# Performance work log

Hardware: AMD Instinct MI355X
Metric: run time of the kernel (lower is better)

Reference implementation:

```python
import jax, jax.numpy as jnp
import numpy as np

# WGS84 constants
_A = 6378137.0
_E2 = 6.69437999014e-3  # first eccentricity squared

ALPHA = 1.0
GAMMA = 2.0
DYNAMIC_GAMMA = True
SCALE_FACTOR = 1.0


def _geodetic_to_ecef(lat_rad, lon_rad, h):
    sl, cl = jnp.sin(lat_rad), jnp.cos(lat_rad)
    so, co = jnp.sin(lon_rad), jnp.cos(lon_rad)
    N = _A / jnp.sqrt(1.0 - _E2 * sl * sl)
    x = (N + h) * cl * co
    y = (N + h) * cl * so
    z = (N * (1.0 - _E2) + h) * sl
    return jnp.stack([x, y, z], axis=-1)


def setup_inputs() -> dict:
    key = jax.random.key(0)
    k1, k2, k3, k4 = jax.random.split(key, 4)
    B = 4_000_000
    lat = jax.random.uniform(k1, (B,), jnp.float32, -80.0, 80.0)    # degrees
    lon = jax.random.uniform(k2, (B,), jnp.float32, -180.0, 180.0)  # degrees
    h = jax.random.uniform(k3, (B,), jnp.float32, 0.0, 1000.0)      # meters
    targets = jnp.stack([lat, lon, h], axis=1)
    ref_ecef = _geodetic_to_ecef(jnp.deg2rad(lat), jnp.deg2rad(lon), h)
    # predicted ECEF = true ECEF + ~meters of noise -> realistic GNSS error
    inputs = ref_ecef + 2.0 * jax.random.normal(k4, (B, 3), jnp.float32)
    return {"inputs": inputs, "targets": targets}


def _ecef_to_enu(pred_ecef, gt_geodetic):
    # Batched version of the per-sample ecef_to_enu_torch loop.
    lat = jnp.deg2rad(gt_geodetic[:, 0])
    lon = jnp.deg2rad(gt_geodetic[:, 1])
    h = gt_geodetic[:, 2]
    ref = _geodetic_to_ecef(lat, lon, h)
    d = pred_ecef - ref  # [B,3]
    sl, cl = jnp.sin(lat), jnp.cos(lat)
    so, co = jnp.sin(lon), jnp.cos(lon)
    dx, dy, dz = d[:, 0], d[:, 1], d[:, 2]
    e = -so * dx + co * dy
    n = -sl * co * dx - sl * so * dy + cl * dz
    u = cl * co * dx + cl * so * dy + sl * dz
    return jnp.stack([e, n, u], axis=1)  # [B,3]


def reference(inputs, targets):
    enu_errors = _ecef_to_enu(inputs, targets)                 # [B,3]
    squared_dist = jnp.sqrt(jnp.sum(enu_errors * enu_errors, axis=1))  # L2 norm [B]
    base_loss = squared_dist
    if DYNAMIC_GAMMA:
        dyn_gamma = GAMMA * jnp.exp(-SCALE_FACTOR * base_loss)
    else:
        dyn_gamma = GAMMA
    focal_weight = jnp.power(1.0 - jnp.sqrt(squared_dist / (jnp.max(squared_dist) + 1e-8)), dyn_gamma)
    focal_loss = ALPHA * focal_weight * base_loss
    return jnp.sqrt(jnp.mean(focal_loss * focal_loss))
```

## Files before the change

kernel.cpp:

```cpp
#include <hip/hip_runtime.h>
#include <hip/hip_fp16.h>
#include <math.h>


#define THREADS 256
#define PART_CAP 8192
#define NB2_CAP 2048
#define BMAX_OFF 64
#define PART_OFF (64 + PART_CAP * 4)
#define DIST_OFF (1 << 20)

__device__ __forceinline__ void sincos8(const double* __restrict__ x,
                                        double* __restrict__ s,
                                        double* __restrict__ c) {
    const double TWO_OVER_PI = 0.636619772367581343076;
    const double PIO2_HI = 1.57079632679489655800e+00;
    const double PIO2_LO = 6.12323399573676603587e-17;

    double kd[8], r[8], r2[8];
    int q[8];
#pragma unroll
    for (int j = 0; j < 8; ++j) {
        kd[j] = rint(x[j] * TWO_OVER_PI);
        q[j] = ((int)kd[j]) & 3;
    }
#pragma unroll
    for (int j = 0; j < 8; ++j) {
        double rr = fma(-kd[j], PIO2_HI, x[j]);
        r[j] = fma(-kd[j], PIO2_LO, rr);
        r2[j] = r[j] * r[j];
    }
    float rf[8], psf[8], pcf[8];
#pragma unroll
    for (int j = 0; j < 8; ++j) rf[j] = (float)r2[j];
#pragma unroll
    for (int j = 0; j < 8; ++j) { psf[j] = -2.50507602534068634195e-08f;
                                  pcf[j] =  2.08757232129817482790e-09f; }
#pragma unroll
    for (int j = 0; j < 8; ++j) { psf[j] = fmaf(psf[j], rf[j],  2.75573137070700676789e-06f);
                                  pcf[j] = fmaf(pcf[j], rf[j], -2.75573143513906633035e-07f); }
#pragma unroll
    for (int j = 0; j < 8; ++j) { psf[j] = fmaf(psf[j], rf[j], -1.98412698298579493134e-04f);
                                  pcf[j] = fmaf(pcf[j], rf[j],  2.48015872894767294178e-05f); }
#pragma unroll
    for (int j = 0; j < 8; ++j) { psf[j] = fmaf(psf[j], rf[j],  8.33333333332248946124e-03f);
                                  pcf[j] = fmaf(pcf[j], rf[j], -1.38888888888741095749e-03f); }
#pragma unroll
    for (int j = 0; j < 8; ++j) {
        double ps = fma((double)psf[j], r2[j], -1.66666666666666324348e-01);
        double pc = fma((double)pcf[j], r2[j],  4.16666666666666019037e-02);
        double sv = fma(r2[j] * r[j], ps, r[j]);
        double cv = fma(r2[j] * r2[j], pc, fma(-0.5, r2[j], 1.0));
        double sr = (q[j] & 1) ? cv : sv;
        double cr = (q[j] & 1) ? sv : cv;
        s[j] = (q[j] & 2) ? -sr : sr;
        c[j] = ((q[j] + 1) & 2) ? -cr : cr;
    }
}

__device__ __forceinline__ void dist_group4(const float* __restrict__ lat,
                                            const float* __restrict__ lon,
                                            const float* __restrict__ hh,
                                            const float* __restrict__ px,
                                            const float* __restrict__ py,
                                            const float* __restrict__ pz,
                                            float* __restrict__ dout) {
    const float D2R = (float)0.017453292519943295;
    double x[8], s8[8], c8[8];
#pragma unroll
    for (int j = 0; j < 4; ++j) x[j] = (double)(lat[j] * D2R);
#pragma unroll
    for (int j = 0; j < 4; ++j) x[4 + j] = (double)(lon[j] * D2R);
    sincos8(x, s8, c8);

    const double A = 6378137.0, E2 = 0.00669437999014;
#pragma unroll
    for (int j = 0; j < 4; ++j) {
        double sl = s8[j], cl = c8[j], so = s8[4 + j], co = c8[4 + j];
        double h = (double)hh[j];
        double w = fma(-E2 * sl, sl, 1.0);
        double y0 = (double)__frsqrt_rn((float)w);
        double y = y0 * fma(-0.5 * w, y0 * y0, 1.5);
        double N = A * y, Nh = N + h;
        double X = Nh * cl * co;
        double Y = Nh * cl * so;
        double Z = fma(N, -E2, N + h) * sl;
        double dx = (double)px[j] - X;
        double dy = (double)py[j] - Y;
        double dz = (double)pz[j] - Z;
        dout[j] = sqrtf((float)(dx * dx + dy * dy + dz * dz));
    }
}

__device__ __forceinline__ float dist_one(float latd, float lond, float hf,
                                          float pxx, float pyy, float pzz) {
    float lat[4] = {latd, latd, latd, latd}, lon[4] = {lond, lond, lond, lond};
    float hh[4] = {hf, hf, hf, hf};
    float px[4] = {pxx, pxx, pxx, pxx}, py[4] = {pyy, pyy, pyy, pyy}, pz[4] = {pzz, pzz, pzz, pzz};
    float d[4];
    dist_group4(lat, lon, hh, px, py, pz, d);
    return d[0];
}

#define UNPACK4(ta, tb, tc, lat, lon, hh)                         \
    float lat[4] = {ta.x, ta.w, tb.z, tc.y};                      \
    float lon[4] = {ta.y, tb.x, tb.w, tc.z};                      \
    float hh[4]  = {ta.z, tb.y, tc.x, tc.w};

__device__ __forceinline__ void store_half4(__half* p, float d0, float d1, float d2, float d3) {
    union { __half2 h2[2]; uint2 u; } pk;
    pk.h2[0] = __floats2half2_rn(d0, d1);
    pk.h2[1] = __floats2half2_rn(d2, d3);
    *(uint2*)p = pk.u;
}

__global__ __launch_bounds__(THREADS, 3)
void k_pass1(const float* __restrict__ inp, const float* __restrict__ tgt,
             __half* __restrict__ dist_arr, float* __restrict__ blockmax, long B) {
    long ngroups = (B + 3) >> 2;
    long nthreads = (long)gridDim.x * blockDim.x;
    long gstride = 2 * nthreads;
    float lmax = 0.0f;
    for (long g = (long)blockIdx.x * blockDim.x + threadIdx.x; g < ngroups; g += gstride) {
        long gA = g;
        long gB = g + nthreads;
        long baseA = gA << 2;
        long baseB = gB << 2;
        bool fastA = (baseA + 3 < B);
        bool fastB = (gB < ngroups) && (baseB + 3 < B);

        if (fastA && fastB) {
            const float4* tA = (const float4*)(tgt + 3 * baseA);
            const float4* pA = (const float4*)(inp + 3 * baseA);
            const float4* tB = (const float4*)(tgt + 3 * baseB);
            const float4* pB = (const float4*)(inp + 3 * baseB);
            float4 ta0 = tA[0], ta1 = tA[1], ta2 = tA[2];
            float4 pa0 = pA[0], pa1 = pA[1], pa2 = pA[2];
            float4 tb0 = tB[0], tb1 = tB[1], tb2 = tB[2];
            float4 pb0 = pB[0], pb1 = pB[1], pb2 = pB[2];

            UNPACK4(ta0, ta1, ta2, latA, lonA, hhA);
            UNPACK4(pa0, pa1, pa2, pxA, pyA, pzA);
            float dA[4];
            dist_group4(latA, lonA, hhA, pxA, pyA, pzA, dA);

            UNPACK4(tb0, tb1, tb2, latB, lonB, hhB);
            UNPACK4(pb0, pb1, pb2, pxB, pyB, pzB);
            float dB[4];
            dist_group4(latB, lonB, hhB, pxB, pyB, pzB, dB);

            if (dist_arr) {
                store_half4(dist_arr + baseA, dA[0], dA[1], dA[2], dA[3]);
                store_half4(dist_arr + baseB, dB[0], dB[1], dB[2], dB[3]);
            }
            lmax = fmaxf(lmax, fmaxf(fmaxf(dA[0], dA[1]), fmaxf(dA[2], dA[3])));
            lmax = fmaxf(lmax, fmaxf(fmaxf(dB[0], dB[1]), fmaxf(dB[2], dB[3])));
        } else {
            for (int pass = 0; pass < 2; ++pass) {
                long gg = pass ? gB : gA;
                if (gg >= ngroups) continue;
                long base = gg << 2;
                long end = base + 4 < B ? base + 4 : B;
                for (long i = base; i < end; ++i) {
                    float d = dist_one(tgt[3*i], tgt[3*i+1], tgt[3*i+2],
                                       inp[3*i], inp[3*i+1], inp[3*i+2]);
                    if (dist_arr) dist_arr[i] = __float2half_rn(d);
                    lmax = fmaxf(lmax, d);
                }
            }
        }
    }
    for (int off = 32; off > 0; off >>= 1)
        lmax = fmaxf(lmax, __shfl_down(lmax, off, 64));
    __shared__ float smax[THREADS / 64];
    if ((threadIdx.x & 63) == 0) smax[threadIdx.x >> 6] = lmax;
    __syncthreads();
    if (threadIdx.x == 0) {
        float m = smax[0];
        for (int w = 1; w < THREADS / 64; ++w) m = fmaxf(m, smax[w]);
        blockmax[blockIdx.x] = m;
    }
}

__device__ __forceinline__ double focal2(float d, float denom) {
    float g = 2.0f * __expf(-d);
    float b = 1.0f - sqrtf(d / denom);
    b = fmaxf(b, 0.0f);
    float wgt = __builtin_amdgcn_exp2f(g * __log2f(b));
    float fl = wgt * d;
    return (double)fl * (double)fl;
}

__global__ void k_pass2(const __half* __restrict__ dist_arr,
                        const float* __restrict__ inp,
                        const float* __restrict__ tgt,
                        const float* __restrict__ blockmax, int nb1,
                        double* __restrict__ partials, long B) {
    __shared__ float smax[THREADS / 64];
    __shared__ double sacc[THREADS / 64];
    __shared__ float sb;
    int tid = threadIdx.x;

    float m = 0.0f;
    for (int i = tid; i < nb1; i += THREADS) m = fmaxf(m, blockmax[i]);
    for (int off = 32; off > 0; off >>= 1)
        m = fmaxf(m, __shfl_down(m, off, 64));
    if ((tid & 63) == 0) smax[tid >> 6] = m;
    __syncthreads();
    if (tid == 0) {
        float mm = smax[0];
        for (int w = 1; w < THREADS / 64; ++w) mm = fmaxf(mm, smax[w]);
        sb = mm;
    }
    __syncthreads();
    float denom = sb + 1e-8f;

    long ngroups = (B + 3) >> 2;
    long gstride = (long)gridDim.x * blockDim.x;
    double acc = 0.0;
    for (long g = (long)blockIdx.x * blockDim.x + tid; g < ngroups; g += gstride) {
        long base = g << 2;
        if (base + 3 < B) {
            float d0, d1, d2, d3;
            if (dist_arr) {
                union { uint2 u; __half2 h2[2]; } pk;
                pk.u = *(const uint2*)(dist_arr + base);
                float2 lo = __half22float2(pk.h2[0]);
                float2 hi = __half22float2(pk.h2[1]);
                d0 = lo.x; d1 = lo.y; d2 = hi.x; d3 = hi.y;
            } else {
                const float4* t4 = (const float4*)(tgt + 3 * base);
                float4 ta = t4[0], tb = t4[1], tc = t4[2];
                const float4* p4 = (const float4*)(inp + 3 * base);
                float4 pa = p4[0], pb = p4[1], pc = p4[2];
                UNPACK4(ta, tb, tc, lat, lon, hh);
                UNPACK4(pa, pb, pc, px, py, pz);
                float d[4];
                dist_group4(lat, lon, hh, px, py, pz, d);
                d0 = d[0]; d1 = d[1]; d2 = d[2]; d3 = d[3];
            }
            acc += focal2(d0, denom) + focal2(d1, denom)
                 + focal2(d2, denom) + focal2(d3, denom);
        } else {
            for (long i = base; i < B; ++i) {
                float d = dist_arr ? __half2float(dist_arr[i])
                                   : dist_one(tgt[3*i], tgt[3*i+1], tgt[3*i+2],
                                              inp[3*i], inp[3*i+1], inp[3*i+2]);
                acc += focal2(d, denom);
            }
        }
    }
    for (int off = 32; off > 0; off >>= 1)
        acc += __shfl_down(acc, off, 64);
    if ((tid & 63) == 0) sacc[tid >> 6] = acc;
    __syncthreads();
    if (tid == 0) {
        double s = sacc[0];
        for (int w = 1; w < THREADS / 64; ++w) s += sacc[w];
        partials[blockIdx.x] = s;
    }
}

__global__ void k_final(const double* __restrict__ partials, int nparts,
                        float* __restrict__ out, long B) {
    double acc = 0.0;
    for (int i = threadIdx.x; i < nparts; i += blockDim.x) acc += partials[i];
    for (int off = 32; off > 0; off >>= 1)
        acc += __shfl_down(acc, off, 64);
    __shared__ double lds[THREADS / 64];
    if ((threadIdx.x & 63) == 0) lds[threadIdx.x >> 6] = acc;
    __syncthreads();
    if (threadIdx.x == 0) {
        double s = lds[0];
        for (int w = 1; w < THREADS / 64; ++w) s += lds[w];
        out[0] = (float)sqrt(s / (double)B);
    }
}

extern "C" void kernel_launch(void* const* d_in, const int* in_sizes, int n_in,
                              void* d_out, int out_size, void* d_ws, size_t ws_size,
                              hipStream_t stream) {
    const float* inp = (const float*)d_in[0];
    const float* tgt = (const float*)d_in[1];
    float* out = (float*)d_out;
    long B = (long)in_sizes[0] / 3;

    float* blockmax = (float*)((char*)d_ws + BMAX_OFF);
    double* partials = (double*)((char*)d_ws + PART_OFF);
    __half* dist_arr = nullptr;
    size_t need = (size_t)DIST_OFF + (size_t)B * sizeof(__half);
    if (ws_size >= need) dist_arr = (__half*)((char*)d_ws + DIST_OFF);

    long ngroups = (B + 3) >> 2;

    long nhalf = (ngroups + 1) >> 1;
    int nb1 = (int)((nhalf + THREADS - 1) / THREADS);
    if (nb1 > PART_CAP) nb1 = PART_CAP;
    if (nb1 < 1) nb1 = 1;

    int nb2 = (int)((ngroups + THREADS - 1) / THREADS);
    if (nb2 > NB2_CAP) nb2 = NB2_CAP;
    if (nb2 < 1) nb2 = 1;

    k_pass1<<<nb1, THREADS, 0, stream>>>(inp, tgt, dist_arr, blockmax, B);
    k_pass2<<<nb2, THREADS, 0, stream>>>(dist_arr, inp, tgt, blockmax, nb1, partials, B);
    k_final<<<1, THREADS, 0, stream>>>(partials, nb2, out, B);
}
```

Measured before the change: 127.2 us.

## Simplify pass1 to one group per thread, float range reduction, reciprocal denom

Pass 1 now handles one 4-point group per thread per iteration instead of two interleaved groups. It doubles the block count and raises the launch-bounds occupancy hint from 3 to 4 to lower register pressure and improve latency hiding. The sincos quadrant reduction computes k in float instead of double, and pass 2 multiplies by a precomputed reciprocal instead of dividing. Doing the quadrant computation in float could round differently for large arguments, and the changes give up the memory-level parallelism of loading two groups at once.

Measured after the change: 128.1 us. Within noise of the previous version (+0.7%).

```diff
diff --git a/kernel.cpp b/kernel.cpp
--- a/kernel.cpp
+++ b/kernel.cpp
@@ -13,7 +13,7 @@
 __device__ __forceinline__ void sincos8(const double* __restrict__ x,
                                         double* __restrict__ s,
                                         double* __restrict__ c) {
-    const double TWO_OVER_PI = 0.636619772367581343076;
+    const float  TWO_OVER_PI_F = 0.636619772367581343076f;
     const double PIO2_HI = 1.57079632679489655800e+00;
     const double PIO2_LO = 6.12323399573676603587e-17;
 
@@ -21,8 +21,9 @@
     int q[8];
 #pragma unroll
     for (int j = 0; j < 8; ++j) {
-        kd[j] = rint(x[j] * TWO_OVER_PI);
-        q[j] = ((int)kd[j]) & 3;
+        float kf = rintf((float)x[j] * TWO_OVER_PI_F);
+        kd[j] = (double)kf;
+        q[j] = ((int)kf) & 3;
     }
 #pragma unroll
     for (int j = 0; j < 8; ++j) {
@@ -82,8 +83,9 @@
         double y0 = (double)__frsqrt_rn((float)w);
         double y = y0 * fma(-0.5 * w, y0 * y0, 1.5);
         double N = A * y, Nh = N + h;
-        double X = Nh * cl * co;
-        double Y = Nh * cl * so;
+        double clh = Nh * cl;
+        double X = clh * co;
+        double Y = clh * so;
         double Z = fma(N, -E2, N + h) * sl;
         double dx = (double)px[j] - X;
         double dy = (double)py[j] - Y;
@@ -114,59 +116,35 @@
     *(uint2*)p = pk.u;
 }
 
-__global__ __launch_bounds__(THREADS, 3)
+__global__ __launch_bounds__(THREADS, 4)
 void k_pass1(const float* __restrict__ inp, const float* __restrict__ tgt,
              __half* __restrict__ dist_arr, float* __restrict__ blockmax, long B) {
     long ngroups = (B + 3) >> 2;
-    long nthreads = (long)gridDim.x * blockDim.x;
-    long gstride = 2 * nthreads;
+    long gstride = (long)gridDim.x * blockDim.x;
     float lmax = 0.0f;
     for (long g = (long)blockIdx.x * blockDim.x + threadIdx.x; g < ngroups; g += gstride) {
-        long gA = g;
-        long gB = g + nthreads;
-        long baseA = gA << 2;
-        long baseB = gB << 2;
-        bool fastA = (baseA + 3 < B);
-        bool fastB = (gB < ngroups) && (baseB + 3 < B);
-
-        if (fastA && fastB) {
-            const float4* tA = (const float4*)(tgt + 3 * baseA);
-            const float4* pA = (const float4*)(inp + 3 * baseA);
-            const float4* tB = (const float4*)(tgt + 3 * baseB);
-            const float4* pB = (const float4*)(inp + 3 * baseB);
-            float4 ta0 = tA[0], ta1 = tA[1], ta2 = tA[2];
-            float4 pa0 = pA[0], pa1 = pA[1], pa2 = pA[2];
-            float4 tb0 = tB[0], tb1 = tB[1], tb2 = tB[2];
-            float4 pb0 = pB[0], pb1 = pB[1], pb2 = pB[2];
-
-            UNPACK4(ta0, ta1, ta2, latA, lonA, hhA);
-            UNPACK4(pa0, pa1, pa2, pxA, pyA, pzA);
-            float dA[4];
-            dist_group4(latA, lonA, hhA, pxA, pyA, pzA, dA);
-
-            UNPACK4(tb0, tb1, tb2, latB, lonB, hhB);
-            UNPACK4(pb0, pb1, pb2, pxB, pyB, pzB);
-            float dB[4];
-            dist_group4(latB, lonB, hhB, pxB, pyB, pzB, dB);
-
-            if (dist_arr) {
-                store_half4(dist_arr + baseA, dA[0], dA[1], dA[2], dA[3]);
-                store_half4(dist_arr + baseB, dB[0], dB[1], dB[2], dB[3]);
-            }
-            lmax = fmaxf(lmax, fmaxf(fmaxf(dA[0], dA[1]), fmaxf(dA[2], dA[3])));
-            lmax = fmaxf(lmax, fmaxf(fmaxf(dB[0], dB[1]), fmaxf(dB[2], dB[3])));
+        long base = g << 2;
+        if (base + 3 < B) {
+            const float4* t4 = (const float4*)(tgt + 3 * base);
+            const float4* p4 = (const float4*)(inp + 3 * base);
+            float4 ta = t4[0], tb = t4[1], tc = t4[2];
+            float4 pa = p4[0], pb = p4[1], pc = p4[2];
+
+            UNPACK4(ta, tb, tc, lat, lon, hh);
+            UNPACK4(pa, pb, pc, px, py, pz);
+            float d[4];
+            dist_group4(lat, lon, hh, px, py, pz, d);
+
+            if (dist_arr)
+                store_half4(dist_arr + base, d[0], d[1], d[2], d[3]);
+            lmax = fmaxf(lmax, fmaxf(fmaxf(d[0], d[1]), fmaxf(d[2], d[3])));
         } else {
-            for (int pass = 0; pass < 2; ++pass) {
-                long gg = pass ? gB : gA;
-                if (gg >= ngroups) continue;
-                long base = gg << 2;
-                long end = base + 4 < B ? base + 4 : B;
-                for (long i = base; i < end; ++i) {
-                    float d = dist_one(tgt[3*i], tgt[3*i+1], tgt[3*i+2],
-                                       inp[3*i], inp[3*i+1], inp[3*i+2]);
-                    if (dist_arr) dist_arr[i] = __float2half_rn(d);
-                    lmax = fmaxf(lmax, d);
-                }
+            long end = base + 4 < B ? base + 4 : B;
+            for (long i = base; i < end; ++i) {
+                float d = dist_one(tgt[3*i], tgt[3*i+1], tgt[3*i+2],
+                                   inp[3*i], inp[3*i+1], inp[3*i+2]);
+                if (dist_arr) dist_arr[i] = __float2half_rn(d);
+                lmax = fmaxf(lmax, d);
             }
         }
     }
@@ -182,9 +160,9 @@
     }
 }
 
-__device__ __forceinline__ double focal2(float d, float denom) {
+__device__ __forceinline__ double focal2(float d, float invden) {
     float g = 2.0f * __expf(-d);
-    float b = 1.0f - sqrtf(d / denom);
+    float b = 1.0f - sqrtf(d * invden);
     b = fmaxf(b, 0.0f);
     float wgt = __builtin_amdgcn_exp2f(g * __log2f(b));
     float fl = wgt * d;
@@ -213,7 +191,7 @@
         sb = mm;
     }
     __syncthreads();
-    float denom = sb + 1e-8f;
+    float invden = 1.0f / (sb + 1e-8f);
 
     long ngroups = (B + 3) >> 2;
     long gstride = (long)gridDim.x * blockDim.x;
@@ -239,14 +217,14 @@
                 dist_group4(lat, lon, hh, px, py, pz, d);
                 d0 = d[0]; d1 = d[1]; d2 = d[2]; d3 = d[3];
             }
-            acc += focal2(d0, denom) + focal2(d1, denom)
-                 + focal2(d2, denom) + focal2(d3, denom);
+            acc += focal2(d0, invden) + focal2(d1, invden)
+                 + focal2(d2, invden) + focal2(d3, invden);
         } else {
             for (long i = base; i < B; ++i) {
                 float d = dist_arr ? __half2float(dist_arr[i])
                                    : dist_one(tgt[3*i], tgt[3*i+1], tgt[3*i+2],
                                               inp[3*i], inp[3*i+1], inp[3*i+2]);
-                acc += focal2(d, denom);
+                acc += focal2(d, invden);
             }
         }
     }
@@ -293,8 +271,7 @@
 
     long ngroups = (B + 3) >> 2;
 
-    long nhalf = (ngroups + 1) >> 1;
-    int nb1 = (int)((nhalf + THREADS - 1) / THREADS);
+    int nb1 = (int)((ngroups + THREADS - 1) / THREADS);
     if (nb1 > PART_CAP) nb1 = PART_CAP;
     if (nb1 < 1) nb1 = 1;
 
```
